# Kernel tuning notes

Measured on AMD Instinct MI355X. Metric: run time of the kernel, lower is better.

Reference implementation:

```python
import jax, jax.numpy as jnp
import numpy as np

N_NODES = 100000
N_EDGES = 1600000
D = 128
BN_EPS = 1e-5


def setup_inputs() -> dict:
    key = jax.random.key(0)
    ks = jax.random.split(key, 6)
    x = jax.random.normal(ks[0], (N_NODES, D), dtype=jnp.float32)
    edge_index = jax.random.randint(ks[1], (2, N_EDGES), 0, N_NODES, dtype=jnp.int64)
    s = 1.0 / np.sqrt(D)
    W1 = jax.random.uniform(ks[2], (D, D), jnp.float32, -s, s)
    W2 = jax.random.uniform(ks[3], (D, D), jnp.float32, -s, s)
    b1 = jnp.zeros((D,), jnp.float32)
    b2 = jnp.zeros((D,), jnp.float32)
    gamma = jnp.ones((D,), jnp.float32)
    beta = jnp.zeros((D,), jnp.float32)
    return {"x": x, "edge_index": edge_index, "W1": W1, "b1": b1,
            "W2": W2, "b2": b2, "gamma": gamma, "beta": beta}


def reference(x, edge_index, W1, b1, W2, b2, gamma, beta):
    src = edge_index[0]
    dst = edge_index[1]
    # GIN aggregation: (1+eps)*x + sum_{j in N(i)} x_j, eps = 0
    agg = jax.ops.segment_sum(x[src], dst, num_segments=x.shape[0])  # [N, D]
    h = agg + x
    # 2-layer MLP
    h = jax.nn.relu(h @ W1 + b1) @ W2 + b2
    # BatchNorm1d (training-mode batch stats, biased variance)
    mean = jnp.mean(h, axis=0)
    var = jnp.mean(jnp.square(h - mean), axis=0)
    h = (h - mean) * jax.lax.rsqrt(var + BN_EPS) * gamma + beta
    # residual; dropout p=0 -> identity
    return h + x
```

## Files before the change

### kernel.cpp

```cpp
#include <hip/hip_runtime.h>
#include <math.h>

#define NNODES 100000
#define NEDGES 1600000
#define DD 128
#define BN_EPS 1e-5f

#define NBUCK 98
#define BUCKW 1024
#define PBLK 500
#define PCHUNK 3200
#define PGRP 800
#define PSTRIDE 512
#define NTILES 1563
#define FMM_GRID 512

typedef __attribute__((ext_vector_type(8))) short bf16x8;
typedef __attribute__((ext_vector_type(4))) float f32x4;
typedef __attribute__((ext_vector_type(4))) unsigned u32x4;

__device__ __forceinline__ unsigned short f2bf(float f) {
  unsigned u = __builtin_bit_cast(unsigned, f);
  u = (u + 0x7fffu + ((u >> 16) & 1u)) >> 16;
  return (unsigned short)u;
}
__device__ __forceinline__ float bfLO(unsigned u) {
  return __builtin_bit_cast(float, u << 16);
}
__device__ __forceinline__ float bfHI(unsigned u) {
  return __builtin_bit_cast(float, u & 0xffff0000u);
}


__global__ __launch_bounds__(256) void k_prep(const float* __restrict__ x,
                                              const float* __restrict__ W1,
                                              const float* __restrict__ W2,
                                              unsigned short* __restrict__ xb,
                                              unsigned short* __restrict__ wt1,
                                              unsigned short* __restrict__ wt2,
                                              float* __restrict__ bnAcc,
                                              const int* __restrict__ e32,
                                              int* __restrict__ cnt) {
  __shared__ int sc[NBUCK];
  int bid = blockIdx.x, tid = threadIdx.x;
  if (bid < 2) {
    const float* W = bid ? W2 : W1;
    unsigned short* wt = bid ? wt2 : wt1;
    if (tid < 128) {
      int n = tid;
      for (int k = 0; k < 128; ++k)
        wt[n * 128 + (k ^ ((n & 7) << 3))] = f2bf(W[k * 128 + n]);
    } else {
      bnAcc[(bid ? 0 : 128) + (tid - 128)] = 0.f;
    }
  } else if (bid < 6252) {
    long j = (long)(bid - 2) * 2048 + tid * 8;
    f32x4 a = __builtin_nontemporal_load((const f32x4*)(x + j));
    f32x4 b = __builtin_nontemporal_load((const f32x4*)(x + j + 4));
    u32x4 o;
    o.x = (unsigned)f2bf(a.x) | ((unsigned)f2bf(a.y) << 16);
    o.y = (unsigned)f2bf(a.z) | ((unsigned)f2bf(a.w) << 16);
    o.z = (unsigned)f2bf(b.x) | ((unsigned)f2bf(b.y) << 16);
    o.w = (unsigned)f2bf(b.z) | ((unsigned)f2bf(b.w) << 16);
    *(u32x4*)(xb + j) = o;
  } else {
    int blk = bid - 6252;
    int z = (tid < 64) ? (e32[2 * tid + 1] == 0) : 1;
    int is64 = __syncthreads_and(z);
    for (int i = tid; i < NBUCK; i += 256) sc[i] = 0;
    __syncthreads();
    const int* dstp = is64 ? (e32 + 2 * (long)NEDGES) : (e32 + NEDGES);
    long e0 = (long)blk * PCHUNK;
    for (int g = tid; g < PGRP; g += 256) {
      long e = e0 + (long)g * 4;
      int d0, d1, d2, d3;
      if (is64) {
        int4 a = *(const int4*)(dstp + 2 * e);
        int4 b = *(const int4*)(dstp + 2 * e + 4);
        d0 = a.x; d1 = a.z; d2 = b.x; d3 = b.z;
      } else {
        int4 a = *(const int4*)(dstp + e);
        d0 = a.x; d1 = a.y; d2 = a.z; d3 = a.w;
      }
      atomicAdd(&sc[d0 >> 10], 1);
      atomicAdd(&sc[d1 >> 10], 1);
      atomicAdd(&sc[d2 >> 10], 1);
      atomicAdd(&sc[d3 >> 10], 1);
    }
    __syncthreads();
    for (int i = tid; i < NBUCK; i += 256) cnt[i * PSTRIDE + blk] = sc[i];
  }
}

__global__ __launch_bounds__(256) void k_lscan(const int* __restrict__ cnt,
                                               int* __restrict__ off,
                                               int* __restrict__ bucketTot) {
  __shared__ int s[256];
  int b = blockIdx.x, tid = threadIdx.x;
  int v0 = (2 * tid < PBLK) ? cnt[b * PSTRIDE + 2 * tid] : 0;
  int v1 = (2 * tid + 1 < PBLK) ? cnt[b * PSTRIDE + 2 * tid + 1] : 0;
  s[tid] = v0 + v1;
  __syncthreads();
  for (int o = 1; o < 256; o <<= 1) {
    int v = (tid >= o) ? s[tid - o] : 0;
    __syncthreads();
    s[tid] += v;
    __syncthreads();
  }
  int excl = s[tid] - v0 - v1;
  off[b * PSTRIDE + 2 * tid] = excl;
  off[b * PSTRIDE + 2 * tid + 1] = excl + v0;
  if (tid == 255) bucketTot[b] = s[255];
}

__global__ __launch_bounds__(256) void k_ppart(const int* __restrict__ e32,
                                               const int* __restrict__ off,
                                               const int* __restrict__ bucketTot,
                                               unsigned* __restrict__ stage) {
  __shared__ int cur[NBUCK];
  __shared__ int sbase[128];
  int tid = threadIdx.x, blk = blockIdx.x;
  int z = (tid < 64) ? (e32[2 * tid + 1] == 0) : 1;
  int is64 = __syncthreads_and(z);
  if (tid < 128) sbase[tid] = (tid < NBUCK) ? bucketTot[tid] : 0;
  __syncthreads();
  for (int o = 1; o < 128; o <<= 1) {
    int v = (tid >= o && tid < 128) ? sbase[tid - o] : 0;
    __syncthreads();
    if (tid < 128) sbase[tid] += v;
    __syncthreads();
  }
  if (tid < NBUCK)
    cur[tid] = off[tid * PSTRIDE + blk] + ((tid == 0) ? 0 : sbase[tid - 1]);
  __syncthreads();
  const int* dstp = is64 ? (e32 + 2 * (long)NEDGES) : (e32 + NEDGES);
  long e0 = (long)blk * PCHUNK;
  for (int g = tid; g < PGRP; g += 256) {
    long e = e0 + (long)g * 4;
    int d0, d1, d2, d3, s0, s1, s2, s3;
    if (is64) {
      int4 da = *(const int4*)(dstp + 2 * e);
      int4 db = *(const int4*)(dstp + 2 * e + 4);
      int4 sa = *(const int4*)(e32 + 2 * e);
      int4 sb = *(const int4*)(e32 + 2 * e + 4);
      d0 = da.x; d1 = da.z; d2 = db.x; d3 = db.z;
      s0 = sa.x; s1 = sa.z; s2 = sb.x; s3 = sb.z;
    } else {
      int4 da = *(const int4*)(dstp + e);
      int4 sa = *(const int4*)(e32 + e);
      d0 = da.x; d1 = da.y; d2 = da.z; d3 = da.w;
      s0 = sa.x; s1 = sa.y; s2 = sa.z; s3 = sa.w;
    }
#define PUT1(dq, sq)                                           \
    {                                                          \
      int pos_ = atomicAdd(&cur[(dq) >> 10], 1);               \
      stage[pos_] = ((unsigned)(sq) << 10) |                   \
                    (unsigned)((dq) & (BUCKW - 1));            \
    }
    PUT1(d0, s0) PUT1(d1, s1) PUT1(d2, s2) PUT1(d3, s3)
#undef PUT1
  }
}

__global__ __launch_bounds__(256) void k_bucket(const unsigned* __restrict__ stage,
                                                const int* __restrict__ bucketTot,
                                                int* __restrict__ rowPtr,
                                                int* __restrict__ edgeSrc) {
  __shared__ int sdeg[BUCKW];
  __shared__ int srow[BUCKW];
  __shared__ int ss[256];
  __shared__ int sbase[128];
  int b = blockIdx.x, tid = threadIdx.x;
  if (tid < 128) sbase[tid] = (tid < NBUCK) ? bucketTot[tid] : 0;
  for (int i = tid; i < BUCKW; i += 256) sdeg[i] = 0;
  __syncthreads();
  for (int o = 1; o < 128; o <<= 1) {
    int v = (tid >= o && tid < 128) ? sbase[tid - o] : 0;
    __syncthreads();
    if (tid < 128) sbase[tid] += v;
    __syncthreads();
  }
  int base = (b == 0) ? 0 : sbase[b - 1];
  int tot = bucketTot[b];
  if (b == 0 && tid == 0) rowPtr[NNODES] = NEDGES;
  const unsigned* st = stage + base;
  for (int i = tid; i < tot; i += 256) atomicAdd(&sdeg[st[i] & (BUCKW - 1)], 1);
  __syncthreads();
  int j = tid * 4;
  int d0 = sdeg[j], d1 = sdeg[j + 1], d2 = sdeg[j + 2], d3 = sdeg[j + 3];
  int tsum = d0 + d1 + d2 + d3;
  ss[tid] = tsum;
  __syncthreads();
  for (int o = 1; o < 256; o <<= 1) {
    int v = (tid >= o) ? ss[tid - o] : 0;
    __syncthreads();
    ss[tid] += v;
    __syncthreads();
  }
  int excl = ss[tid] - tsum;
  srow[j] = excl;
  srow[j + 1] = excl + d0;
  srow[j + 2] = excl + d0 + d1;
  srow[j + 3] = excl + d0 + d1 + d2;
  __syncthreads();
  for (int i = tid; i < BUCKW; i += 256) {
    int dst = b * BUCKW + i;
    if (dst < NNODES) rowPtr[dst] = base + srow[i];
    sdeg[i] = srow[i];
  }
  __syncthreads();
  for (int i = tid; i < tot; i += 256) {
    unsigned p = st[i];
    int pos = atomicAdd(&sdeg[p & (BUCKW - 1)], 1);
    edgeSrc[base + pos] = (int)(p >> 10);
  }
}

__global__ __launch_bounds__(256) void k_gather(const u32x4* __restrict__ xb4,
                                                const int* __restrict__ rowPtr,
                                                const int* __restrict__ edgeSrc,
                                                u32x4* __restrict__ h0b4) {
  int node = (blockIdx.x * 256 + threadIdx.x) >> 6;
  int lane = threadIdx.x & 63;
  if (node >= NNODES) return;
  int li = lane & 15, q = lane >> 4;
  int beg = rowPtr[node], end = rowPtr[node + 1];
  float a0 = 0.f, a1 = 0.f, a2 = 0.f, a3 = 0.f;
  float a4 = 0.f, a5 = 0.f, a6 = 0.f, a7 = 0.f;
#define ACC8(v)                                              \
  a0 += bfLO((v).x); a1 += bfHI((v).x);                      \
  a2 += bfLO((v).y); a3 += bfHI((v).y);                      \
  a4 += bfLO((v).z); a5 += bfHI((v).z);                      \
  a6 += bfLO((v).w); a7 += bfHI((v).w);
  if (q == 0) {
    u32x4 u = xb4[(long)node * 16 + li];
    ACC8(u)
  }
  int e = beg;
  for (; e + 16 <= end; e += 16) {
    int s0 = edgeSrc[e + q];
    int s1 = edgeSrc[e + 4 + q];
    int s2 = edgeSrc[e + 8 + q];
    int s3 = edgeSrc[e + 12 + q];
    u32x4 v0 = xb4[(long)s0 * 16 + li];
    u32x4 v1 = xb4[(long)s1 * 16 + li];
    u32x4 v2 = xb4[(long)s2 * 16 + li];
    u32x4 v3 = xb4[(long)s3 * 16 + li];
    ACC8(v0) ACC8(v1) ACC8(v2) ACC8(v3)
  }
  if (e + 8 <= end) {
    int s0 = edgeSrc[e + q];
    int s1 = edgeSrc[e + 4 + q];
    u32x4 v0 = xb4[(long)s0 * 16 + li];
    u32x4 v1 = xb4[(long)s1 * 16 + li];
    ACC8(v0) ACC8(v1)
    e += 8;
  }
  for (; e < end; e += 4) {
    if (q < end - e) {
      int s = edgeSrc[e + q];
      u32x4 v = xb4[(long)s * 16 + li];
      ACC8(v)
    }
  }
#undef ACC8
  a0 += __shfl_xor(a0, 16, 64); a0 += __shfl_xor(a0, 32, 64);
  a1 += __shfl_xor(a1, 16, 64); a1 += __shfl_xor(a1, 32, 64);
  a2 += __shfl_xor(a2, 16, 64); a2 += __shfl_xor(a2, 32, 64);
  a3 += __shfl_xor(a3, 16, 64); a3 += __shfl_xor(a3, 32, 64);
  a4 += __shfl_xor(a4, 16, 64); a4 += __shfl_xor(a4, 32, 64);
  a5 += __shfl_xor(a5, 16, 64); a5 += __shfl_xor(a5, 32, 64);
  a6 += __shfl_xor(a6, 16, 64); a6 += __shfl_xor(a6, 32, 64);
  a7 += __shfl_xor(a7, 16, 64); a7 += __shfl_xor(a7, 32, 64);
  if (q == 0) {
    u32x4 o;
    o.x = (unsigned)f2bf(a0) | ((unsigned)f2bf(a1) << 16);
    o.y = (unsigned)f2bf(a2) | ((unsigned)f2bf(a3) << 16);
    o.z = (unsigned)f2bf(a4) | ((unsigned)f2bf(a5) << 16);
    o.w = (unsigned)f2bf(a6) | ((unsigned)f2bf(a7) << 16);
    h0b4[(long)node * 16 + li] = o;
  }
}

__global__ __launch_bounds__(256) void k_fmm(const unsigned short* Ab,
                                             const unsigned short* __restrict__ Wt1,
                                             const unsigned short* __restrict__ Wt2,
                                             const float* __restrict__ b1,
                                             const float* __restrict__ b2,
                                             unsigned short* Cb,
                                             float* __restrict__ bnSum,
                                             float* __restrict__ bnSq) {
  __shared__ __align__(16) char smem[81920];
  unsigned short* sW1 = (unsigned short*)smem;
  unsigned short* sW2 = (unsigned short*)(smem + 32768);
  unsigned short* sH  = (unsigned short*)(smem + 65536);
  float* sbn = (float*)(smem + 65536);
  int tid = threadIdx.x;
#pragma unroll
  for (int i = 0; i < 8; ++i) {
    ((u32x4*)sW1)[tid + 256 * i] = ((const u32x4*)Wt1)[tid + 256 * i];
    ((u32x4*)sW2)[tid + 256 * i] = ((const u32x4*)Wt2)[tid + 256 * i];
  }
  int w = tid >> 6, lane = tid & 63, l4 = lane >> 4, l15 = lane & 15;
  float bb1[8], bb2[8], ls[8], lq[8];
#pragma unroll
  for (int ni = 0; ni < 8; ++ni) {
    bb1[ni] = b1[ni * 16 + l15];
    bb2[ni] = b2[ni * 16 + l15];
    ls[ni] = 0.f; lq[ni] = 0.f;
  }

  int tile = blockIdx.x;
  bf16x8 af[4];
  {
    int r = tile * 64 + w * 16 + l15;
    if (r > NNODES - 1) r = NNODES - 1;
#pragma unroll
    for (int ks = 0; ks < 4; ++ks)
      af[ks] = __builtin_nontemporal_load(
          (const bf16x8*)(Ab + (long)r * 128 + ks * 32 + l4 * 8));
  }
  __syncthreads();

  while (tile < NTILES) {
    int next = tile + FMM_GRID;
    f32x4 acc[8];
#pragma unroll
    for (int ni = 0; ni < 8; ++ni) acc[ni] = (f32x4){0.f, 0.f, 0.f, 0.f};
#pragma unroll
    for (int ks = 0; ks < 4; ++ks)
#pragma unroll
      for (int ni = 0; ni < 8; ++ni) {
        int n = ni * 16 + l15, k = ks * 32 + l4 * 8;
        bf16x8 bf = *(const bf16x8*)(sW1 + n * 128 + (k ^ ((n & 7) << 3)));
        acc[ni] = __builtin_amdgcn_mfma_f32_16x16x32_bf16(af[ks], bf, acc[ni], 0, 0, 0);
      }
    __syncthreads();
#pragma unroll
    for (int ni = 0; ni < 8; ++ni) {
      int col = ni * 16 + l15;
#pragma unroll
      for (int rr = 0; rr < 4; ++rr) {
        int row = w * 16 + l4 * 4 + rr;
        float v = fmaxf(acc[ni][rr] + bb1[ni], 0.f);
        sH[row * 128 + (col ^ ((row & 7) << 3))] = f2bf(v);
      }
    }
    __syncthreads();
    bf16x8 afn[4] = {af[0], af[1], af[2], af[3]};
    if (next < NTILES) {
      int r = next * 64 + w * 16 + l15;
      if (r > NNODES - 1) r = NNODES - 1;
#pragma unroll
      for (int ks = 0; ks < 4; ++ks)
        afn[ks] = __builtin_nontemporal_load(
            (const bf16x8*)(Ab + (long)r * 128 + ks * 32 + l4 * 8));
    }
    bf16x8 a2[4];
    {
      int row = w * 16 + l15;
#pragma unroll
      for (int ks = 0; ks < 4; ++ks) {
        int k = ks * 32 + l4 * 8;
        a2[ks] = *(const bf16x8*)(sH + row * 128 + (k ^ ((row & 7) << 3)));
      }
    }
#pragma unroll
    for (int ni = 0; ni < 8; ++ni) acc[ni] = (f32x4){0.f, 0.f, 0.f, 0.f};
#pragma unroll
    for (int ks = 0; ks < 4; ++ks)
#pragma unroll
      for (int ni = 0; ni < 8; ++ni) {
        int n = ni * 16 + l15, k = ks * 32 + l4 * 8;
        bf16x8 bf = *(const bf16x8*)(sW2 + n * 128 + (k ^ ((n & 7) << 3)));
        acc[ni] = __builtin_amdgcn_mfma_f32_16x16x32_bf16(a2[ks], bf, acc[ni], 0, 0, 0);
      }
#pragma unroll
    for (int ni = 0; ni < 8; ++ni) {
      int n = ni * 16 + l15;
#pragma unroll
      for (int rr = 0; rr < 4; ++rr) {
        int row = tile * 64 + w * 16 + l4 * 4 + rr;
        if (row < NNODES) {
          float v = acc[ni][rr] + bb2[ni];
          __builtin_nontemporal_store(f2bf(v), Cb + (long)row * 128 + n);
          ls[ni] += v; lq[ni] += v * v;
        }
      }
    }
#pragma unroll
    for (int ks = 0; ks < 4; ++ks) af[ks] = afn[ks];
    tile = next;
  }

#pragma unroll
  for (int j = 0; j < 8; ++j) {
    ls[j] += __shfl_xor(ls[j], 16, 64); ls[j] += __shfl_xor(ls[j], 32, 64);
    lq[j] += __shfl_xor(lq[j], 16, 64); lq[j] += __shfl_xor(lq[j], 32, 64);
  }
  __syncthreads();
  if (l4 == 0) {
#pragma unroll
    for (int j = 0; j < 8; ++j) {
      sbn[w * 256 + j * 16 + l15] = ls[j];
      sbn[w * 256 + 128 + j * 16 + l15] = lq[j];
    }
  }
  __syncthreads();
  {
    float t = sbn[tid] + sbn[256 + tid] + sbn[512 + tid] + sbn[768 + tid];
    if (tid < 128) atomicAdd(&bnSum[tid], t);
    else atomicAdd(&bnSq[tid - 128], t);
  }
}

__global__ __launch_bounds__(256) void k_epi(const u32x4* __restrict__ h2b4,
                                             const u32x4* __restrict__ xb4,
                                             const float* __restrict__ bnSum,
                                             const float* __restrict__ bnSq,
                                             const float* __restrict__ gamma,
                                             const float* __restrict__ beta,
                                             f32x4* __restrict__ out4) {
  __shared__ float ssc[128], ssh[128];
  int tid = threadIdx.x;
  if (tid < 128) {
    float m = bnSum[tid] * (1.0f / NNODES);
    float var = bnSq[tid] * (1.0f / NNODES) - m * m;
    float sc = gamma[tid] * rsqrtf(var + BN_EPS);
    ssc[tid] = sc;
    ssh[tid] = beta[tid] - m * sc;
  }
  __syncthreads();
  long j = (long)blockIdx.x * 256 + tid;
  int c = (int)((j * 8) & 127);
  u32x4 h = __builtin_nontemporal_load(h2b4 + j);
  u32x4 xr = __builtin_nontemporal_load(xb4 + j);
  f32x4 sa = *(f32x4*)(ssc + c), sb = *(f32x4*)(ssc + c + 4);
  f32x4 fa = *(f32x4*)(ssh + c), fb = *(f32x4*)(ssh + c + 4);
  f32x4 oa, ob;
  oa.x = fmaf(bfLO(h.x), sa.x, fa.x) + bfLO(xr.x);
  oa.y = fmaf(bfHI(h.x), sa.y, fa.y) + bfHI(xr.x);
  oa.z = fmaf(bfLO(h.y), sa.z, fa.z) + bfLO(xr.y);
  oa.w = fmaf(bfHI(h.y), sa.w, fa.w) + bfHI(xr.y);
  ob.x = fmaf(bfLO(h.z), sb.x, fb.x) + bfLO(xr.z);
  ob.y = fmaf(bfHI(h.z), sb.y, fb.y) + bfHI(xr.z);
  ob.z = fmaf(bfLO(h.w), sb.z, fb.z) + bfLO(xr.w);
  ob.w = fmaf(bfHI(h.w), sb.w, fb.w) + bfHI(xr.w);
  __builtin_nontemporal_store(oa, out4 + 2 * j);
  __builtin_nontemporal_store(ob, out4 + 2 * j + 1);
}

extern "C" void kernel_launch(void* const* d_in, const int* in_sizes, int n_in,
                              void* d_out, int out_size, void* d_ws, size_t ws_size,
                              hipStream_t stream) {
  const float* x     = (const float*)d_in[0];
  const int*   e32   = (const int*)d_in[1];
  const float* W1    = (const float*)d_in[2];
  const float* b1    = (const float*)d_in[3];
  const float* W2    = (const float*)d_in[4];
  const float* b2    = (const float*)d_in[5];
  const float* gamma = (const float*)d_in[6];
  const float* beta  = (const float*)d_in[7];
  float* out = (float*)d_out;

  char* ws = (char*)d_ws;
  const size_t BFB = (size_t)NNODES * DD * 2;
  unsigned short* xb  = (unsigned short*)ws;
  unsigned short* h0b = (unsigned short*)(ws + BFB);
  unsigned short* h2b = h0b;

  int* rowPtr     = (int*)(ws + 3 * BFB);
  int* edgeSrc    = rowPtr + NNODES + 4;
  unsigned* stage = (unsigned*)(edgeSrc + NEDGES);
  int* cnt        = (int*)(stage + NEDGES);
  int* off        = cnt + NBUCK * PSTRIDE;
  int* bucketTot  = off + NBUCK * PSTRIDE;

  unsigned short* wt1 = (unsigned short*)(bucketTot + 256);
  unsigned short* wt2 = wt1 + 16384;
  float* bnSum = (float*)(wt2 + 16384);
  float* bnSq  = bnSum + 128;

  k_prep<<<6252 + PBLK, 256, 0, stream>>>(x, W1, W2, xb, wt1, wt2, bnSum, e32,
                                          cnt);
  k_lscan<<<NBUCK, 256, 0, stream>>>(cnt, off, bucketTot);
  k_ppart<<<PBLK, 256, 0, stream>>>(e32, off, bucketTot, stage);
  k_bucket<<<NBUCK, 256, 0, stream>>>(stage, bucketTot, rowPtr, edgeSrc);
  k_gather<<<25000, 256, 0, stream>>>((const u32x4*)xb, rowPtr, edgeSrc,
                                      (u32x4*)h0b);
  k_fmm<<<FMM_GRID, 256, 0, stream>>>(h0b, wt1, wt2, b1, b2, h2b, bnSum, bnSq);
  k_epi<<<6250, 256, 0, stream>>>((const u32x4*)h2b, (const u32x4*)xb, bnSum,
                                  bnSq, gamma, beta, (f32x4*)out);
}
```

Baseline: 196.5 us.

## Replace count/scan partition with atomic bucket reservation; read W2 from global in fused MLP

The separate histogram pass in prep and the per-block scan kernel are removed. Each partition block now counts its own bucket histogram and reserves slots with a global atomicAdd into fixed-capacity per-bucket regions of the staging buffer, which drops one kernel launch and the count/offset arrays. In the fused MLP kernel, W2 is no longer staged in shared memory; it is read straight from global/L2, which cuts LDS use so more blocks can be resident, and the grid grows from 512 to 768 to match. The risks are that within-bucket order becomes nondeterministic, that a bucket holding more than BCAP edges would overflow, and that every W2 fragment now costs a global load.

Measured after the change: 212.4 us. 1.08x slower.

```diff
diff --git a/kernel.cpp b/kernel.cpp
--- a/kernel.cpp
+++ b/kernel.cpp
@@ -8,12 +8,12 @@
 
 #define NBUCK 98
 #define BUCKW 1024
+#define BCAP 20480
 #define PBLK 500
 #define PCHUNK 3200
 #define PGRP 800
-#define PSTRIDE 512
 #define NTILES 1563
-#define FMM_GRID 512
+#define FMM_GRID 768
 
 typedef __attribute__((ext_vector_type(8))) short bf16x8;
 typedef __attribute__((ext_vector_type(4))) float f32x4;
@@ -39,9 +39,7 @@
                                               unsigned short* __restrict__ wt1,
                                               unsigned short* __restrict__ wt2,
                                               float* __restrict__ bnAcc,
-                                              const int* __restrict__ e32,
-                                              int* __restrict__ cnt) {
-  __shared__ int sc[NBUCK];
+                                              int* __restrict__ bucketCur) {
   int bid = blockIdx.x, tid = threadIdx.x;
   if (bid < 2) {
     const float* W = bid ? W2 : W1;
@@ -53,7 +51,8 @@
     } else {
       bnAcc[(bid ? 0 : 128) + (tid - 128)] = 0.f;
     }
-  } else if (bid < 6252) {
+  } else {
+    if (bid == 2 && tid < 128) bucketCur[tid] = 0;
     long j = (long)(bid - 2) * 2048 + tid * 8;
     f32x4 a = __builtin_nontemporal_load((const f32x4*)(x + j));
     f32x4 b = __builtin_nontemporal_load((const f32x4*)(x + j + 4));
@@ -63,78 +62,41 @@
     o.z = (unsigned)f2bf(b.x) | ((unsigned)f2bf(b.y) << 16);
     o.w = (unsigned)f2bf(b.z) | ((unsigned)f2bf(b.w) << 16);
     *(u32x4*)(xb + j) = o;
-  } else {
-    int blk = bid - 6252;
-    int z = (tid < 64) ? (e32[2 * tid + 1] == 0) : 1;
-    int is64 = __syncthreads_and(z);
-    for (int i = tid; i < NBUCK; i += 256) sc[i] = 0;
-    __syncthreads();
-    const int* dstp = is64 ? (e32 + 2 * (long)NEDGES) : (e32 + NEDGES);
-    long e0 = (long)blk * PCHUNK;
-    for (int g = tid; g < PGRP; g += 256) {
-      long e = e0 + (long)g * 4;
-      int d0, d1, d2, d3;
-      if (is64) {
-        int4 a = *(const int4*)(dstp + 2 * e);
-        int4 b = *(const int4*)(dstp + 2 * e + 4);
-        d0 = a.x; d1 = a.z; d2 = b.x; d3 = b.z;
-      } else {
-        int4 a = *(const int4*)(dstp + e);
-        d0 = a.x; d1 = a.y; d2 = a.z; d3 = a.w;
-      }
-      atomicAdd(&sc[d0 >> 10], 1);
-      atomicAdd(&sc[d1 >> 10], 1);
-      atomicAdd(&sc[d2 >> 10], 1);
-      atomicAdd(&sc[d3 >> 10], 1);
-    }
-    __syncthreads();
-    for (int i = tid; i < NBUCK; i += 256) cnt[i * PSTRIDE + blk] = sc[i];
-  }
-}
-
-__global__ __launch_bounds__(256) void k_lscan(const int* __restrict__ cnt,
-                                               int* __restrict__ off,
-                                               int* __restrict__ bucketTot) {
-  __shared__ int s[256];
-  int b = blockIdx.x, tid = threadIdx.x;
-  int v0 = (2 * tid < PBLK) ? cnt[b * PSTRIDE + 2 * tid] : 0;
-  int v1 = (2 * tid + 1 < PBLK) ? cnt[b * PSTRIDE + 2 * tid + 1] : 0;
-  s[tid] = v0 + v1;
-  __syncthreads();
-  for (int o = 1; o < 256; o <<= 1) {
-    int v = (tid >= o) ? s[tid - o] : 0;
-    __syncthreads();
-    s[tid] += v;
-    __syncthreads();
-  }
-  int excl = s[tid] - v0 - v1;
-  off[b * PSTRIDE + 2 * tid] = excl;
-  off[b * PSTRIDE + 2 * tid + 1] = excl + v0;
-  if (tid == 255) bucketTot[b] = s[255];
+  }
 }
 
 __global__ __launch_bounds__(256) void k_ppart(const int* __restrict__ e32,
-                                               const int* __restrict__ off,
-                                               const int* __restrict__ bucketTot,
+                                               int* __restrict__ bucketCur,
                                                unsigned* __restrict__ stage) {
+  __shared__ int sc[NBUCK];
   __shared__ int cur[NBUCK];
-  __shared__ int sbase[128];
   int tid = threadIdx.x, blk = blockIdx.x;
   int z = (tid < 64) ? (e32[2 * tid + 1] == 0) : 1;
   int is64 = __syncthreads_and(z);
-  if (tid < 128) sbase[tid] = (tid < NBUCK) ? bucketTot[tid] : 0;
-  __syncthreads();
-  for (int o = 1; o < 128; o <<= 1) {
-    int v = (tid >= o && tid < 128) ? sbase[tid - o] : 0;
-    __syncthreads();
-    if (tid < 128) sbase[tid] += v;
-    __syncthreads();
-  }
-  if (tid < NBUCK)
-    cur[tid] = off[tid * PSTRIDE + blk] + ((tid == 0) ? 0 : sbase[tid - 1]);
+  for (int i = tid; i < NBUCK; i += 256) sc[i] = 0;
   __syncthreads();
   const int* dstp = is64 ? (e32 + 2 * (long)NEDGES) : (e32 + NEDGES);
   long e0 = (long)blk * PCHUNK;
+  for (int g = tid; g < PGRP; g += 256) {
+    long e = e0 + (long)g * 4;
+    int d0, d1, d2, d3;
+    if (is64) {
+      int4 a = *(const int4*)(dstp + 2 * e);
+      int4 b = *(const int4*)(dstp + 2 * e + 4);
+      d0 = a.x; d1 = a.z; d2 = b.x; d3 = b.z;
+    } else {
+      int4 a = *(const int4*)(dstp + e);
+      d0 = a.x; d1 = a.y; d2 = a.z; d3 = a.w;
+    }
+    atomicAdd(&sc[d0 >> 10], 1);
+    atomicAdd(&sc[d1 >> 10], 1);
+    atomicAdd(&sc[d2 >> 10], 1);
+    atomicAdd(&sc[d3 >> 10], 1);
+  }
+  __syncthreads();
+  for (int i = tid; i < NBUCK; i += 256)
+    cur[i] = atomicAdd(&bucketCur[i], sc[i]);
+  __syncthreads();
   for (int g = tid; g < PGRP; g += 256) {
     long e = e0 + (long)g * 4;
     int d0, d1, d2, d3, s0, s1, s2, s3;
@@ -151,11 +113,12 @@
       d0 = da.x; d1 = da.y; d2 = da.z; d3 = da.w;
       s0 = sa.x; s1 = sa.y; s2 = sa.z; s3 = sa.w;
     }
-#define PUT1(dq, sq)                                           \
-    {                                                          \
-      int pos_ = atomicAdd(&cur[(dq) >> 10], 1);               \
-      stage[pos_] = ((unsigned)(sq) << 10) |                   \
-                    (unsigned)((dq) & (BUCKW - 1));            \
+#define PUT1(dq, sq)                                             \
+    {                                                            \
+      int bkt_ = (dq) >> 10;                                     \
+      int pos_ = atomicAdd(&cur[bkt_], 1);                       \
+      stage[(long)bkt_ * BCAP + pos_] =                          \
+          ((unsigned)(sq) << 10) | (unsigned)((dq) & (BUCKW - 1)); \
     }
     PUT1(d0, s0) PUT1(d1, s1) PUT1(d2, s2) PUT1(d3, s3)
 #undef PUT1
@@ -163,7 +126,7 @@
 }
 
 __global__ __launch_bounds__(256) void k_bucket(const unsigned* __restrict__ stage,
-                                                const int* __restrict__ bucketTot,
+                                                const int* __restrict__ bucketCur,
                                                 int* __restrict__ rowPtr,
                                                 int* __restrict__ edgeSrc) {
   __shared__ int sdeg[BUCKW];
@@ -171,7 +134,7 @@
   __shared__ int ss[256];
   __shared__ int sbase[128];
   int b = blockIdx.x, tid = threadIdx.x;
-  if (tid < 128) sbase[tid] = (tid < NBUCK) ? bucketTot[tid] : 0;
+  if (tid < 128) sbase[tid] = (tid < NBUCK) ? bucketCur[tid] : 0;
   for (int i = tid; i < BUCKW; i += 256) sdeg[i] = 0;
   __syncthreads();
   for (int o = 1; o < 128; o <<= 1) {
@@ -181,9 +144,9 @@
     __syncthreads();
   }
   int base = (b == 0) ? 0 : sbase[b - 1];
-  int tot = bucketTot[b];
+  int tot = bucketCur[b];
   if (b == 0 && tid == 0) rowPtr[NNODES] = NEDGES;
-  const unsigned* st = stage + base;
+  const unsigned* st = stage + (long)b * BCAP;
   for (int i = tid; i < tot; i += 256) atomicAdd(&sdeg[st[i] & (BUCKW - 1)], 1);
   __syncthreads();
   int j = tid * 4;
@@ -290,17 +253,14 @@
                                              unsigned short* Cb,
                                              float* __restrict__ bnSum,
                                              float* __restrict__ bnSq) {
-  __shared__ __align__(16) char smem[81920];
+  __shared__ __align__(16) char smem[49152];
   unsigned short* sW1 = (unsigned short*)smem;
-  unsigned short* sW2 = (unsigned short*)(smem + 32768);
-  unsigned short* sH  = (unsigned short*)(smem + 65536);
-  float* sbn = (float*)(smem + 65536);
+  unsigned short* sH  = (unsigned short*)(smem + 32768);
+  float* sbn = (float*)(smem + 32768);
   int tid = threadIdx.x;
 #pragma unroll
-  for (int i = 0; i < 8; ++i) {
+  for (int i = 0; i < 8; ++i)
     ((u32x4*)sW1)[tid + 256 * i] = ((const u32x4*)Wt1)[tid + 256 * i];
-    ((u32x4*)sW2)[tid + 256 * i] = ((const u32x4*)Wt2)[tid + 256 * i];
-  }
   int w = tid >> 6, lane = tid & 63, l4 = lane >> 4, l15 = lane & 15;
   float bb1[8], bb2[8], ls[8], lq[8];
 #pragma unroll
@@ -372,7 +332,7 @@
 #pragma unroll
       for (int ni = 0; ni < 8; ++ni) {
         int n = ni * 16 + l15, k = ks * 32 + l4 * 8;
-        bf16x8 bf = *(const bf16x8*)(sW2 + n * 128 + (k ^ ((n & 7) << 3)));
+        bf16x8 bf = *(const bf16x8*)(Wt2 + n * 128 + (k ^ ((n & 7) << 3)));
         acc[ni] = __builtin_amdgcn_mfma_f32_16x16x32_bf16(a2[ks], bf, acc[ni], 0, 0, 0);
       }
 #pragma unroll
@@ -469,23 +429,19 @@
   unsigned short* h0b = (unsigned short*)(ws + BFB);
   unsigned short* h2b = h0b;
 
-  int* rowPtr     = (int*)(ws + 3 * BFB);
-  int* edgeSrc    = rowPtr + NNODES + 4;
-  unsigned* stage = (unsigned*)(edgeSrc + NEDGES);
-  int* cnt        = (int*)(stage + NEDGES);
-  int* off        = cnt + NBUCK * PSTRIDE;
-  int* bucketTot  = off + NBUCK * PSTRIDE;
-
-  unsigned short* wt1 = (unsigned short*)(bucketTot + 256);
+  int* rowPtr       = (int*)(ws + 3 * BFB);
+  int* edgeSrc      = rowPtr + NNODES + 4;
+  unsigned* stage   = (unsigned*)(edgeSrc + NEDGES);
+  int* bucketCur    = (int*)(stage + (long)NBUCK * BCAP);
+
+  unsigned short* wt1 = (unsigned short*)(bucketCur + 128);
   unsigned short* wt2 = wt1 + 16384;
   float* bnSum = (float*)(wt2 + 16384);
   float* bnSq  = bnSum + 128;
 
-  k_prep<<<6252 + PBLK, 256, 0, stream>>>(x, W1, W2, xb, wt1, wt2, bnSum, e32,
-                                          cnt);
-  k_lscan<<<NBUCK, 256, 0, stream>>>(cnt, off, bucketTot);
-  k_ppart<<<PBLK, 256, 0, stream>>>(e32, off, bucketTot, stage);
-  k_bucket<<<NBUCK, 256, 0, stream>>>(stage, bucketTot, rowPtr, edgeSrc);
+  k_prep<<<6252, 256, 0, stream>>>(x, W1, W2, xb, wt1, wt2, bnSum, bucketCur);
+  k_ppart<<<PBLK, 256, 0, stream>>>(e32, bucketCur, stage);
+  k_bucket<<<NBUCK, 256, 0, stream>>>(stage, bucketCur, rowPtr, edgeSrc);
   k_gather<<<25000, 256, 0, stream>>>((const u32x4*)xb, rowPtr, edgeSrc,
                                       (u32x4*)h0b);
   k_fmm<<<FMM_GRID, 256, 0, stream>>>(h0b, wt1, wt2, b1, b2, h2b, bnSum, bnSq);
```
